# Performance work log

Hardware: AMD Instinct MI355X
Metric: run time of the kernel (lower is better)

The kernel has to match this reference:

```python
import math
import jax, jax.numpy as jnp
import numpy as np

B, S, D, H = 4, 2048, 768, 8


def setup_inputs() -> dict:
    key = jax.random.key(0)
    ks = jax.random.split(key, 8)
    x = jax.random.normal(ks[0], (B, S, D), dtype=jnp.float32)
    # padding mask: True = masked position, shape [B, S, 1] as consumed by forward
    attention_mask = jax.random.randint(ks[1], (B, S, 1), 0, 2) == 1
    W_q = jax.random.normal(ks[2], (D, D), dtype=jnp.float32) * 0.02
    b_q = jax.random.normal(ks[3], (D,), dtype=jnp.float32) * 0.02
    W_v = jax.random.normal(ks[4], (D, D), dtype=jnp.float32) * 0.02
    b_v = jax.random.normal(ks[5], (D,), dtype=jnp.float32) * 0.02
    gamma = jnp.ones((D,), dtype=jnp.float32)
    beta = jnp.zeros((D,), dtype=jnp.float32)
    return {"x": x, "attention_mask": attention_mask, "W_q": W_q, "b_q": b_q,
            "W_v": W_v, "b_v": b_v, "gamma": gamma, "beta": beta}


def reference(x, attention_mask, W_q, b_q, W_v, b_v, gamma, beta):
    b, s, d = x.shape
    dk = d // H
    scale = math.sqrt(dk)
    q = (x @ W_q.T + b_q).reshape(b, s, H, dk).transpose(0, 2, 1, 3)  # [B,H,S,dk]
    # faithful to source: k and v BOTH use the V projection (original bug)
    kv = (x @ W_v.T + b_v).reshape(b, s, H, dk).transpose(0, 2, 1, 3)
    k = kv
    v = kv
    weight = jnp.einsum('bhid,bhjd->bhij', q, k) / scale  # [B,H,S,S]
    pad = attention_mask[:, None, :, :]                   # [B,1,S,1] -> broadcast over heads, j
    causal = jnp.triu(jnp.ones((s, s), dtype=bool), 1)    # [S,S]
    mask = pad | causal
    weight = jnp.where(mask, jnp.float32(-1e9), weight)
    # faithful: softmax over dim=2 (the query axis), as in the source
    score = jax.nn.softmax(weight, axis=2)
    out = jnp.einsum('bhij,bhjd->bhid', score, v)         # [B,H,S,dk]
    out = out.transpose(0, 2, 1, 3).reshape(b, s, d)
    out = out + x                                          # residual
    mu = jnp.mean(out, axis=-1, keepdims=True)
    var = jnp.mean((out - mu) ** 2, axis=-1, keepdims=True)
    return (out - mu) / jnp.sqrt(var + 1e-5) * gamma + beta
```

## Files before the change

### kernel.cpp

```cpp
#include <hip/hip_runtime.h>

#define B 4
#define S 2048
#define D 768
#define H 8
#define DK 96
#define NBH (B*H)
#define SD (B*S*D)

typedef __bf16 bf16x8 __attribute__((ext_vector_type(8)));
typedef float f32x4 __attribute__((ext_vector_type(4)));
typedef unsigned short ushort_t;
typedef __attribute__((ext_vector_type(8))) unsigned short ushort8;
typedef __attribute__((ext_vector_type(4))) unsigned short us4;

static constexpr float INV_SCALE = 0.10206207261596577f;
static constexpr float NEG = -1.0e9f;

__device__ __forceinline__ ushort_t f2bf(float f) {
    union { float f; unsigned u; } v; v.f = f;
    unsigned r = v.u + 0x7fffu + ((v.u >> 16) & 1u);
    return (ushort_t)(r >> 16);
}

__device__ __forceinline__ unsigned cvt_pk(float a, float b) {
    unsigned d;
    asm("v_cvt_pk_bf16_f32 %0, %1, %2" : "=v"(d) : "v"(a), "v"(b));
    return d;
}
__device__ __forceinline__ ushort8 pack8(const float4& a, const float4& b) {
    union { unsigned u[4]; ushort8 s; } r;
    r.u[0] = cvt_pk(a.x, a.y); r.u[1] = cvt_pk(a.z, a.w);
    r.u[2] = cvt_pk(b.x, b.y); r.u[3] = cvt_pk(b.z, b.w);
    return r.s;
}
__device__ __forceinline__ us4 pack4(const float4& a) {
    union { unsigned u[2]; us4 s; } r;
    r.u[0] = cvt_pk(a.x, a.y); r.u[1] = cvt_pk(a.z, a.w);
    return r.s;
}

#define MFMA16(a, b, c) __builtin_amdgcn_mfma_f32_16x16x32_bf16((a), (b), (c), 0, 0, 0)

__global__ __launch_bounds__(256) void convert_bf16(
    const float* __restrict__ wq, const float* __restrict__ wv,
    ushort_t* __restrict__ wqb, ushort_t* __restrict__ wvb)
{
    const int stride = gridDim.x * 256;
    const int idx = blockIdx.x * 256 + threadIdx.x;
    for (int i = idx; i < (D * D) / 4; i += stride) {
        ((us4*)wqb)[i] = pack4(((const float4*)wq)[i]);
        ((us4*)wvb)[i] = pack4(((const float4*)wv)[i]);
    }
}

__global__ __launch_bounds__(256) void in_proj_gemm(
    const float* __restrict__ x,
    const ushort_t* __restrict__ wqb, const float* __restrict__ bq,
    const ushort_t* __restrict__ wvb, const float* __restrict__ bv,
    ushort_t* __restrict__ Qb, ushort_t* __restrict__ KVb,
    ushort_t* __restrict__ KVt)
{
    const ushort_t* __restrict__ Wm = blockIdx.z ? wvb : wqb;
    const float* __restrict__ bia   = blockIdx.z ? bv : bq;
    ushort_t* __restrict__ outp     = blockIdx.z ? KVb : Qb;

    const int bn = blockIdx.x * 128;
    const int bm = blockIdx.y * 128;
    const int tid = threadIdx.x;
    const int lane = tid & 63;
    const int wid = tid >> 6;
    const int wm = (wid >> 1) * 64, wn = (wid & 1) * 64;
    const int lr = lane & 15, lg = lane >> 4;

    __shared__ __align__(16) ushort_t As[2][128][40];
    __shared__ __align__(16) ushort_t Bs[2][128][40];

    const int r0 = tid >> 2, c8 = (tid & 3) * 8;
    const float*    xg0 = &x [(size_t)(bm + r0) * D + c8];
    const float*    xg1 = xg0 + (size_t)64 * D;
    const ushort_t* wg0 = &Wm[(size_t)(bn + r0) * D + c8];
    const ushort_t* wg1 = wg0 + (size_t)64 * D;

    float4 xv[4];
    ushort8 wv2[2];

    f32x4 acc[4][4];
    #pragma unroll
    for (int m = 0; m < 4; ++m)
        #pragma unroll
        for (int n = 0; n < 4; ++n) acc[m][n] = (f32x4){0.f, 0.f, 0.f, 0.f};

    {
        xv[0] = *(const float4*)(xg0);     xv[1] = *(const float4*)(xg0 + 4);
        xv[2] = *(const float4*)(xg1);     xv[3] = *(const float4*)(xg1 + 4);
        wv2[0] = *(const ushort8*)(wg0);   wv2[1] = *(const ushort8*)(wg1);
        *(ushort8*)&As[0][r0][c8]      = pack8(xv[0], xv[1]);
        *(ushort8*)&As[0][r0 + 64][c8] = pack8(xv[2], xv[3]);
        *(ushort8*)&Bs[0][r0][c8]      = wv2[0];
        *(ushort8*)&Bs[0][r0 + 64][c8] = wv2[1];
    }

    for (int k = 0; k < 24; ++k) {
        __syncthreads();
        const int buf = k & 1;
        if (k < 23) {
            const int ko = (k + 1) * 32;
            xv[0] = *(const float4*)(xg0 + ko);     xv[1] = *(const float4*)(xg0 + ko + 4);
            xv[2] = *(const float4*)(xg1 + ko);     xv[3] = *(const float4*)(xg1 + ko + 4);
            wv2[0] = *(const ushort8*)(wg0 + ko);   wv2[1] = *(const ushort8*)(wg1 + ko);
        }
        bf16x8 a[4], bfr[4];
        #pragma unroll
        for (int m = 0; m < 4; ++m) a[m]   = *(const bf16x8*)&As[buf][wm + m * 16 + lr][lg * 8];
        #pragma unroll
        for (int n = 0; n < 4; ++n) bfr[n] = *(const bf16x8*)&Bs[buf][wn + n * 16 + lr][lg * 8];
        #pragma unroll
        for (int m = 0; m < 4; ++m)
            #pragma unroll
            for (int n = 0; n < 4; ++n)
                acc[m][n] = MFMA16(a[m], bfr[n], acc[m][n]);
        if (k < 23) {
            const int nb = (k + 1) & 1;
            *(ushort8*)&As[nb][r0][c8]      = pack8(xv[0], xv[1]);
            *(ushort8*)&As[nb][r0 + 64][c8] = pack8(xv[2], xv[3]);
            *(ushort8*)&Bs[nb][r0][c8]      = wv2[0];
            *(ushort8*)&Bs[nb][r0 + 64][c8] = wv2[1];
        }
    }

    #pragma unroll
    for (int m = 0; m < 4; ++m) {
        #pragma unroll
        for (int n = 0; n < 4; ++n) {
            int col = bn + wn + n * 16 + lr;
            float bb = bia[col];
            int row0 = bm + wm + m * 16 + lg * 4;
            us4 o;
            #pragma unroll
            for (int r = 0; r < 4; ++r) o[r] = f2bf(acc[m][n][r] + bb);
            #pragma unroll
            for (int r = 0; r < 4; ++r) outp[(size_t)(row0 + r) * D + col] = o[r];
            if (blockIdx.z) {
                int hh = col / DK, dd = col - hh * DK;
                int bb2 = row0 >> 11, ss = row0 & (S - 1);
                *(us4*)&KVt[((size_t)(bb2 * H + hh) * DK + dd) * S + ss] = o;
            }
        }
    }
}

__global__ __launch_bounds__(256) void col_stats(
    const ushort_t* __restrict__ Qb, const ushort_t* __restrict__ KVb,
    const int* __restrict__ amask,
    float* __restrict__ colM, float* __restrict__ colSinv)
{
    const int bh = blockIdx.y;
    const int jt = (blockIdx.x + 8 * ((bh >> 3) & 3)) & 31;
    const int b = bh >> 3, h = bh & 7;
    const int j0 = jt * 64;
    const int tid = threadIdx.x;
    const int lane = tid & 63;
    const int w = tid >> 6;
    const int lr = lane & 15, lg = lane >> 4;

    __shared__ __align__(16) ushort_t qs[2][64][104];
    __shared__ int pads[2][64];

    bf16x8 kf[3];
    #pragma unroll
    for (int ks2 = 0; ks2 < 3; ++ks2)
        kf[ks2] = *(const bf16x8*)&KVb[(size_t)(b * S + j0 + w * 16 + lr) * D + h * DK + ks2 * 32 + lg * 8];

    int kr[3], kc[3];
    const ushort_t* qg[3];
    #pragma unroll
    for (int k3 = 0; k3 < 3; ++k3) {
        int c = tid + k3 * 256;
        kr[k3] = c / 12; kc[k3] = (c % 12) * 8;
        qg[k3] = &Qb[(size_t)(b * S + j0 + kr[k3]) * D + h * DK + kc[k3]];
    }
    const int* pg = amask + b * S + j0 + (tid < 64 ? tid : 0);

    ushort8 pq[3]; int ppad = 0;
    #pragma unroll
    for (int k3 = 0; k3 < 3; ++k3) { pq[k3] = *(const ushort8*)qg[k3]; qg[k3] += (size_t)64 * D; }
    if (tid < 64) { ppad = *pg; }
    pg += 64;

    float m = NEG, ssum = 0.f;
    const int jg = j0 + w * 16 + lr;
    const int nit = (S / 64) - jt;

    for (int t = 0; t < nit; ++t) {
        const int buf = t & 1;
        const int i0 = j0 + t * 64;
        #pragma unroll
        for (int k3 = 0; k3 < 3; ++k3) *(ushort8*)&qs[buf][kr[k3]][kc[k3]] = pq[k3];
        if (tid < 64) pads[buf][tid] = ppad;
        __syncthreads();
        if (t + 1 < nit) {
            #pragma unroll
            for (int k3 = 0; k3 < 3; ++k3) { pq[k3] = *(const ushort8*)qg[k3]; qg[k3] += (size_t)64 * D; }
            if (tid < 64) { ppad = *pg; }
            pg += 64;
        }

        f32x4 dacc[4];
        #pragma unroll
        for (int f = 0; f < 4; ++f) dacc[f] = (f32x4){0.f, 0.f, 0.f, 0.f};
        #pragma unroll
        for (int ks2 = 0; ks2 < 3; ++ks2) {
            #pragma unroll
            for (int f = 0; f < 4; ++f) {
                bf16x8 afr = *(const bf16x8*)&qs[buf][f * 16 + lr][ks2 * 32 + lg * 8];
                dacc[f] = MFMA16(afr, kf[ks2], dacc[f]);
            }
        }

        #pragma unroll
        for (int f = 0; f < 4; ++f) {
            const int ib = f * 16 + lg * 4;
            float wv[4];
            #pragma unroll
            for (int r = 0; r < 4; ++r) {
                int ig = i0 + ib + r;
                wv[r] = (pads[buf][ib + r] != 0 || jg > ig) ? NEG : dacc[f][r] * INV_SCALE;
            }
            float vmax = fmaxf(fmaxf(wv[0], wv[1]), fmaxf(wv[2], wv[3]));
            float mn = fmaxf(m, vmax);
            ssum = ssum * __expf(m - mn)
                 + __expf(wv[0] - mn) + __expf(wv[1] - mn)
                 + __expf(wv[2] - mn) + __expf(wv[3] - mn);
            m = mn;
        }
    }

    float m2 = m, s2 = ssum;
    #pragma unroll
    for (int off = 16; off < 64; off <<= 1) {
        float mo = __shfl_xor(m2, off);
        float so = __shfl_xor(s2, off);
        float mn = fmaxf(m2, mo);
        s2 = s2 * __expf(m2 - mn) + so * __expf(mo - mn);
        m2 = mn;
    }
    if (lane < 16) {
        if (m2 == NEG) s2 += (float)j0;
        colM[bh * S + jg] = m2;
        colSinv[bh * S + jg] = 1.0f / s2;
    }
}

__global__ __launch_bounds__(256, 4) void attn_pv(
    const ushort_t* __restrict__ Qb, const ushort_t* __restrict__ KVb,
    const ushort_t* __restrict__ KVt,
    const int* __restrict__ amask,
    const float* __restrict__ colM, const float* __restrict__ colSinv,
    const float* __restrict__ x, float* __restrict__ out)
{
    const int bh = blockIdx.y;
    const int it = (blockIdx.x + 8 * ((bh >> 3) & 3)) & 31;
    const int b = bh >> 3, h = bh & 7;
    const int i0 = it * 64;
    const int tid = threadIdx.x;
    const int lane = tid & 63;
    const int w = tid >> 6;
    const int lr = lane & 15, lg = lane >> 4;

    __shared__ __align__(16) ushort_t kvs[64][104];
    __shared__ __align__(16) ushort_t kvt[96][72];
    __shared__ __align__(16) ushort_t ps[64][72];
    __shared__ __align__(16) float cm[64];
    __shared__ __align__(16) float csv[64];
    __shared__ int padi[64];

    bf16x8 qf[3];
    #pragma unroll
    for (int ks2 = 0; ks2 < 3; ++ks2)
        qf[ks2] = *(const bf16x8*)&Qb[(size_t)(b * S + i0 + w * 16 + lr) * D + h * DK + ks2 * 32 + lg * 8];

    if (tid < 64) padi[tid] = amask[b * S + i0 + tid];

    int kr[3], kc[3], tr[3], tc[3];
    const ushort_t* kvg[3];
    const ushort_t* ktg[3];
    #pragma unroll
    for (int k3 = 0; k3 < 3; ++k3) {
        int c = tid + k3 * 256;
        kr[k3] = c / 12;  kc[k3] = (c % 12) * 8;
        tr[k3] = c >> 3;  tc[k3] = (c & 7) * 8;
        kvg[k3] = &KVb[(size_t)(b * S + kr[k3]) * D + h * DK + kc[k3]];
        ktg[k3] = &KVt[((size_t)(b * H + h) * DK + tr[k3]) * S + tc[k3]];
    }
    const float* cmg  = colM    + (size_t)bh * S + (tid < 64 ? tid : 0);
    const float* csvg = colSinv + (size_t)bh * S + (tid < 64 ? tid : 0);

    ushort8 pkv[3], pkt[3]; float pcm = 0.f, pcsv = 0.f;
    #pragma unroll
    for (int k3 = 0; k3 < 3; ++k3) {
        pkv[k3] = *(const ushort8*)kvg[k3];  kvg[k3] += (size_t)64 * D;
        pkt[k3] = *(const ushort8*)ktg[k3];  ktg[k3] += 64;
    }
    if (tid < 64) { pcm = *cmg; pcsv = *csvg; }
    cmg += 64; csvg += 64;

    f32x4 acc[6];
    #pragma unroll
    for (int df = 0; df < 6; ++df) acc[df] = (f32x4){0.f, 0.f, 0.f, 0.f};

    const int my_pad = (int)(amask[b * S + i0 + w * 16 + lr] != 0);
    const int i_g = i0 + w * 16 + lr;

    for (int jt2 = 0; jt2 <= it; ++jt2) {
        const int j0 = jt2 * 64;
        __syncthreads();
        #pragma unroll
        for (int k3 = 0; k3 < 3; ++k3) {
            *(ushort8*)&kvs[kr[k3]][kc[k3]] = pkv[k3];
            *(ushort8*)&kvt[tr[k3]][tc[k3]] = pkt[k3];
        }
        if (tid < 64) { cm[tid] = pcm; csv[tid] = pcsv; }
        __syncthreads();
        if (jt2 < it) {
            #pragma unroll
            for (int k3 = 0; k3 < 3; ++k3) {
                pkv[k3] = *(const ushort8*)kvg[k3];  kvg[k3] += (size_t)64 * D;
                pkt[k3] = *(const ushort8*)ktg[k3];  ktg[k3] += 64;
            }
            if (tid < 64) { pcm = *cmg; pcsv = *csvg; }
            cmg += 64; csvg += 64;
        }

        f32x4 dacc[4];
        #pragma unroll
        for (int jf = 0; jf < 4; ++jf) dacc[jf] = (f32x4){0.f, 0.f, 0.f, 0.f};
        #pragma unroll
        for (int ks2 = 0; ks2 < 3; ++ks2) {
            #pragma unroll
            for (int jf = 0; jf < 4; ++jf) {
                bf16x8 afr = *(const bf16x8*)&kvs[jf * 16 + lr][ks2 * 32 + lg * 8];
                dacc[jf] = MFMA16(afr, qf[ks2], dacc[jf]);
            }
        }

        #pragma unroll
        for (int jf = 0; jf < 4; ++jf) {
            const int jbase = jf * 16 + lg * 4;
            f32x4 cmv  = *(const f32x4*)&cm[jbase];
            f32x4 csvv = *(const f32x4*)&csv[jbase];
            float pv[4];
            #pragma unroll
            for (int r = 0; r < 4; ++r) {
                int jgl = j0 + jbase + r;
                bool msk = my_pad || (jgl > i_g);
                float wvv = msk ? NEG : dacc[jf][r] * INV_SCALE;
                pv[r] = __expf(wvv - cmv[r]) * csvv[r];
            }
            union { unsigned u[2]; uint2 v; } o;
            o.u[0] = cvt_pk(pv[0], pv[1]);
            o.u[1] = cvt_pk(pv[2], pv[3]);
            *(uint2*)&ps[w * 16 + lr][jbase] = o.v;
        }

        #pragma unroll
        for (int ks2 = 0; ks2 < 2; ++ks2) {
            bf16x8 afr = *(const bf16x8*)&ps[w * 16 + lr][ks2 * 32 + lg * 8];
            #pragma unroll
            for (int df = 0; df < 6; ++df) {
                bf16x8 bfr = *(const bf16x8*)&kvt[df * 16 + lr][ks2 * 32 + lg * 8];
                acc[df] = MFMA16(afr, bfr, acc[df]);
            }
        }
    }

    #pragma unroll
    for (int df = 0; df < 6; ++df) {
        int d = h * DK + df * 16 + lr;
        #pragma unroll
        for (int r = 0; r < 4; ++r) {
            size_t gi = (size_t)(b * S + i0 + w * 16 + lg * 4 + r) * D + d;
            out[gi] = acc[df][r] + x[gi];
        }
    }
}

__global__ __launch_bounds__(256) void layer_norm(
    float* __restrict__ out,
    const float* __restrict__ gamma, const float* __restrict__ beta)
{
    const int row = blockIdx.x * 4 + (threadIdx.x >> 6);
    const int lane = threadIdx.x & 63;
    float* o = out + (size_t)row * D;

    float4 v[3];
    #pragma unroll
    for (int p = 0; p < 3; ++p) v[p] = *(const float4*)&o[lane * 4 + p * 256];

    float s = 0.f;
    #pragma unroll
    for (int p = 0; p < 3; ++p) s += v[p].x + v[p].y + v[p].z + v[p].w;
    #pragma unroll
    for (int off = 1; off < 64; off <<= 1) s += __shfl_xor(s, off);
    const float mu = s * (1.0f / D);

    float q = 0.f;
    #pragma unroll
    for (int p = 0; p < 3; ++p) {
        float a = v[p].x - mu, bb = v[p].y - mu, c = v[p].z - mu, dd = v[p].w - mu;
        q += a * a + bb * bb + c * c + dd * dd;
    }
    #pragma unroll
    for (int off = 1; off < 64; off <<= 1) q += __shfl_xor(q, off);
    const float inv = 1.0f / sqrtf(q * (1.0f / D) + 1e-5f);

    #pragma unroll
    for (int p = 0; p < 3; ++p) {
        float4 g = *(const float4*)&gamma[lane * 4 + p * 256];
        float4 bt = *(const float4*)&beta[lane * 4 + p * 256];
        float4 r;
        r.x = (v[p].x - mu) * inv * g.x + bt.x;
        r.y = (v[p].y - mu) * inv * g.y + bt.y;
        r.z = (v[p].z - mu) * inv * g.z + bt.z;
        r.w = (v[p].w - mu) * inv * g.w + bt.w;
        *(float4*)&o[lane * 4 + p * 256] = r;
    }
}

extern "C" void kernel_launch(void* const* d_in, const int* in_sizes, int n_in,
                              void* d_out, int out_size, void* d_ws, size_t ws_size,
                              hipStream_t stream)
{
    const float* x     = (const float*)d_in[0];
    const int*   amask = (const int*)  d_in[1];
    const float* Wq    = (const float*)d_in[2];
    const float* bq    = (const float*)d_in[3];
    const float* Wv    = (const float*)d_in[4];
    const float* bv    = (const float*)d_in[5];
    const float* gamma = (const float*)d_in[6];
    const float* beta  = (const float*)d_in[7];
    float* out = (float*)d_out;

    ushort_t* wqb  = (ushort_t*)d_ws;
    ushort_t* wvb  = wqb + (size_t)D * D;
    ushort_t* Qb   = wvb + (size_t)D * D;
    ushort_t* KVb  = Qb  + (size_t)SD;
    ushort_t* KVt  = KVb + (size_t)SD;
    float* colM    = (float*)(KVt + (size_t)SD);
    float* colSinv = colM + (size_t)NBH * S;

    convert_bf16<<<576, 256, 0, stream>>>(Wq, Wv, wqb, wvb);
    in_proj_gemm<<<dim3(D / 128, (B * S) / 128, 2), 256, 0, stream>>>(
        x, wqb, bq, wvb, bv, Qb, KVb, KVt);
    col_stats<<<dim3(S / 64, NBH), 256, 0, stream>>>(
        Qb, KVb, amask, colM, colSinv);
    attn_pv<<<dim3(S / 64, NBH), 256, 0, stream>>>(
        Qb, KVb, KVt, amask, colM, colSinv, x, out);
    layer_norm<<<(B * S) / 4, 256, 0, stream>>>(out, gamma, beta);
}
```

Baseline: 178.1 us.

## Load attention operands straight from global into registers and fold scale into Q

Both attention kernels stop staging Q/K/V tiles, mask and column stats through shared memory with double buffering and block barriers. Each wave now loads its MFMA fragments directly from global memory (relying on L2/cache reuse across waves) and drops the __syncthreads. The softmax scale times log2(e) is folded into the Q projection epilogue so the kernels use raw exp2 instead of multiply plus __expf. Launch bounds change too; the risk is redundant global traffic across the four waves and higher register pressure.

```diff
diff --git a/kernel.cpp b/kernel.cpp
--- a/kernel.cpp
+++ b/kernel.cpp
@@ -14,8 +14,10 @@
 typedef __attribute__((ext_vector_type(8))) unsigned short ushort8;
 typedef __attribute__((ext_vector_type(4))) unsigned short us4;
 
-static constexpr float INV_SCALE = 0.10206207261596577f;
 static constexpr float NEG = -1.0e9f;
+static constexpr float SCALE_L2E = 0.14724515567714155f;
+
+__device__ __forceinline__ float exp2v(float x) { return __builtin_amdgcn_exp2f(x); }
 
 __device__ __forceinline__ ushort_t f2bf(float f) {
     union { float f; unsigned u; } v; v.f = f;
@@ -64,6 +66,7 @@
     const ushort_t* __restrict__ Wm = blockIdx.z ? wvb : wqb;
     const float* __restrict__ bia   = blockIdx.z ? bv : bq;
     ushort_t* __restrict__ outp     = blockIdx.z ? KVb : Qb;
+    const float osc = blockIdx.z ? 1.0f : SCALE_L2E;
 
     const int bn = blockIdx.x * 128;
     const int bm = blockIdx.y * 128;
@@ -138,7 +141,7 @@
             int row0 = bm + wm + m * 16 + lg * 4;
             us4 o;
             #pragma unroll
-            for (int r = 0; r < 4; ++r) o[r] = f2bf(acc[m][n][r] + bb);
+            for (int r = 0; r < 4; ++r) o[r] = f2bf((acc[m][n][r] + bb) * osc);
             #pragma unroll
             for (int r = 0; r < 4; ++r) outp[(size_t)(row0 + r) * D + col] = o[r];
             if (blockIdx.z) {
@@ -150,7 +153,7 @@
     }
 }
 
-__global__ __launch_bounds__(256) void col_stats(
+__global__ __launch_bounds__(256, 4) void col_stats(
     const ushort_t* __restrict__ Qb, const ushort_t* __restrict__ KVb,
     const int* __restrict__ amask,
     float* __restrict__ colM, float* __restrict__ colSinv)
@@ -159,79 +162,61 @@
     const int jt = (blockIdx.x + 8 * ((bh >> 3) & 3)) & 31;
     const int b = bh >> 3, h = bh & 7;
     const int j0 = jt * 64;
-    const int tid = threadIdx.x;
-    const int lane = tid & 63;
-    const int w = tid >> 6;
+    const int lane = threadIdx.x & 63;
+    const int w = threadIdx.x >> 6;
     const int lr = lane & 15, lg = lane >> 4;
-
-    __shared__ __align__(16) ushort_t qs[2][64][104];
-    __shared__ int pads[2][64];
 
     bf16x8 kf[3];
     #pragma unroll
     for (int ks2 = 0; ks2 < 3; ++ks2)
         kf[ks2] = *(const bf16x8*)&KVb[(size_t)(b * S + j0 + w * 16 + lr) * D + h * DK + ks2 * 32 + lg * 8];
 
-    int kr[3], kc[3];
-    const ushort_t* qg[3];
-    #pragma unroll
-    for (int k3 = 0; k3 < 3; ++k3) {
-        int c = tid + k3 * 256;
-        kr[k3] = c / 12; kc[k3] = (c % 12) * 8;
-        qg[k3] = &Qb[(size_t)(b * S + j0 + kr[k3]) * D + h * DK + kc[k3]];
-    }
-    const int* pg = amask + b * S + j0 + (tid < 64 ? tid : 0);
-
-    ushort8 pq[3]; int ppad = 0;
-    #pragma unroll
-    for (int k3 = 0; k3 < 3; ++k3) { pq[k3] = *(const ushort8*)qg[k3]; qg[k3] += (size_t)64 * D; }
-    if (tid < 64) { ppad = *pg; }
-    pg += 64;
+    const ushort_t* qbase = &Qb[(size_t)(b * S + j0 + lr) * D + h * DK + lg * 8];
+    const int* pbase = &amask[b * S + j0 + lg * 4];
 
     float m = NEG, ssum = 0.f;
     const int jg = j0 + w * 16 + lr;
     const int nit = (S / 64) - jt;
 
     for (int t = 0; t < nit; ++t) {
-        const int buf = t & 1;
         const int i0 = j0 + t * 64;
-        #pragma unroll
-        for (int k3 = 0; k3 < 3; ++k3) *(ushort8*)&qs[buf][kr[k3]][kc[k3]] = pq[k3];
-        if (tid < 64) pads[buf][tid] = ppad;
-        __syncthreads();
-        if (t + 1 < nit) {
-            #pragma unroll
-            for (int k3 = 0; k3 < 3; ++k3) { pq[k3] = *(const ushort8*)qg[k3]; qg[k3] += (size_t)64 * D; }
-            if (tid < 64) { ppad = *pg; }
-            pg += 64;
-        }
+        const ushort_t* qt = qbase + (size_t)t * 64 * D;
+        const int* pt = pbase + t * 64;
+
+        bf16x8 af[4][3];
+        #pragma unroll
+        for (int f = 0; f < 4; ++f)
+            #pragma unroll
+            for (int ks2 = 0; ks2 < 3; ++ks2)
+                af[f][ks2] = *(const bf16x8*)(qt + (size_t)f * 16 * D + ks2 * 32);
+        int4 pd4[4];
+        #pragma unroll
+        for (int f = 0; f < 4; ++f) pd4[f] = *(const int4*)(pt + f * 16);
 
         f32x4 dacc[4];
         #pragma unroll
         for (int f = 0; f < 4; ++f) dacc[f] = (f32x4){0.f, 0.f, 0.f, 0.f};
         #pragma unroll
-        for (int ks2 = 0; ks2 < 3; ++ks2) {
-            #pragma unroll
-            for (int f = 0; f < 4; ++f) {
-                bf16x8 afr = *(const bf16x8*)&qs[buf][f * 16 + lr][ks2 * 32 + lg * 8];
-                dacc[f] = MFMA16(afr, kf[ks2], dacc[f]);
-            }
-        }
+        for (int ks2 = 0; ks2 < 3; ++ks2)
+            #pragma unroll
+            for (int f = 0; f < 4; ++f)
+                dacc[f] = MFMA16(af[f][ks2], kf[ks2], dacc[f]);
 
         #pragma unroll
         for (int f = 0; f < 4; ++f) {
             const int ib = f * 16 + lg * 4;
+            const int* pd = (const int*)&pd4[f];
             float wv[4];
             #pragma unroll
             for (int r = 0; r < 4; ++r) {
                 int ig = i0 + ib + r;
-                wv[r] = (pads[buf][ib + r] != 0 || jg > ig) ? NEG : dacc[f][r] * INV_SCALE;
+                wv[r] = (pd[r] != 0 || jg > ig) ? NEG : dacc[f][r];
             }
             float vmax = fmaxf(fmaxf(wv[0], wv[1]), fmaxf(wv[2], wv[3]));
             float mn = fmaxf(m, vmax);
-            ssum = ssum * __expf(m - mn)
-                 + __expf(wv[0] - mn) + __expf(wv[1] - mn)
-                 + __expf(wv[2] - mn) + __expf(wv[3] - mn);
+            ssum = ssum * exp2v(m - mn)
+                 + exp2v(wv[0] - mn) + exp2v(wv[1] - mn)
+                 + exp2v(wv[2] - mn) + exp2v(wv[3] - mn);
             m = mn;
         }
     }
@@ -242,7 +227,7 @@
         float mo = __shfl_xor(m2, off);
         float so = __shfl_xor(s2, off);
         float mn = fmaxf(m2, mo);
-        s2 = s2 * __expf(m2 - mn) + so * __expf(mo - mn);
+        s2 = s2 * exp2v(m2 - mn) + so * exp2v(mo - mn);
         m2 = mn;
     }
     if (lane < 16) {
@@ -252,7 +237,7 @@
     }
 }
 
-__global__ __launch_bounds__(256, 4) void attn_pv(
+__global__ __launch_bounds__(256, 3) void attn_pv(
     const ushort_t* __restrict__ Qb, const ushort_t* __restrict__ KVb,
     const ushort_t* __restrict__ KVt,
     const int* __restrict__ amask,
@@ -263,99 +248,73 @@
     const int it = (blockIdx.x + 8 * ((bh >> 3) & 3)) & 31;
     const int b = bh >> 3, h = bh & 7;
     const int i0 = it * 64;
-    const int tid = threadIdx.x;
-    const int lane = tid & 63;
-    const int w = tid >> 6;
+    const int lane = threadIdx.x & 63;
+    const int w = threadIdx.x >> 6;
     const int lr = lane & 15, lg = lane >> 4;
 
-    __shared__ __align__(16) ushort_t kvs[64][104];
-    __shared__ __align__(16) ushort_t kvt[96][72];
     __shared__ __align__(16) ushort_t ps[64][72];
-    __shared__ __align__(16) float cm[64];
-    __shared__ __align__(16) float csv[64];
-    __shared__ int padi[64];
 
     bf16x8 qf[3];
     #pragma unroll
     for (int ks2 = 0; ks2 < 3; ++ks2)
         qf[ks2] = *(const bf16x8*)&Qb[(size_t)(b * S + i0 + w * 16 + lr) * D + h * DK + ks2 * 32 + lg * 8];
 
-    if (tid < 64) padi[tid] = amask[b * S + i0 + tid];
-
-    int kr[3], kc[3], tr[3], tc[3];
-    const ushort_t* kvg[3];
-    const ushort_t* ktg[3];
-    #pragma unroll
-    for (int k3 = 0; k3 < 3; ++k3) {
-        int c = tid + k3 * 256;
-        kr[k3] = c / 12;  kc[k3] = (c % 12) * 8;
-        tr[k3] = c >> 3;  tc[k3] = (c & 7) * 8;
-        kvg[k3] = &KVb[(size_t)(b * S + kr[k3]) * D + h * DK + kc[k3]];
-        ktg[k3] = &KVt[((size_t)(b * H + h) * DK + tr[k3]) * S + tc[k3]];
-    }
-    const float* cmg  = colM    + (size_t)bh * S + (tid < 64 ? tid : 0);
-    const float* csvg = colSinv + (size_t)bh * S + (tid < 64 ? tid : 0);
-
-    ushort8 pkv[3], pkt[3]; float pcm = 0.f, pcsv = 0.f;
-    #pragma unroll
-    for (int k3 = 0; k3 < 3; ++k3) {
-        pkv[k3] = *(const ushort8*)kvg[k3];  kvg[k3] += (size_t)64 * D;
-        pkt[k3] = *(const ushort8*)ktg[k3];  ktg[k3] += 64;
-    }
-    if (tid < 64) { pcm = *cmg; pcsv = *csvg; }
-    cmg += 64; csvg += 64;
-
-    f32x4 acc[6];
-    #pragma unroll
-    for (int df = 0; df < 6; ++df) acc[df] = (f32x4){0.f, 0.f, 0.f, 0.f};
-
     const int my_pad = (int)(amask[b * S + i0 + w * 16 + lr] != 0);
     const int i_g = i0 + w * 16 + lr;
 
+    const ushort_t* kbase = &KVb[(size_t)(b * S + lr) * D + h * DK + lg * 8];
+    const ushort_t* vbase = &KVt[((size_t)(b * H + h) * DK + lr) * S + lg * 8];
+    const float* cmb  = colM    + (size_t)bh * S + lg * 4;
+    const float* csvb = colSinv + (size_t)bh * S + lg * 4;
+
+    f32x4 acc[6];
+    #pragma unroll
+    for (int df = 0; df < 6; ++df) acc[df] = (f32x4){0.f, 0.f, 0.f, 0.f};
+
     for (int jt2 = 0; jt2 <= it; ++jt2) {
         const int j0 = jt2 * 64;
-        __syncthreads();
-        #pragma unroll
-        for (int k3 = 0; k3 < 3; ++k3) {
-            *(ushort8*)&kvs[kr[k3]][kc[k3]] = pkv[k3];
-            *(ushort8*)&kvt[tr[k3]][tc[k3]] = pkt[k3];
-        }
-        if (tid < 64) { cm[tid] = pcm; csv[tid] = pcsv; }
-        __syncthreads();
-        if (jt2 < it) {
-            #pragma unroll
-            for (int k3 = 0; k3 < 3; ++k3) {
-                pkv[k3] = *(const ushort8*)kvg[k3];  kvg[k3] += (size_t)64 * D;
-                pkt[k3] = *(const ushort8*)ktg[k3];  ktg[k3] += 64;
-            }
-            if (tid < 64) { pcm = *cmg; pcsv = *csvg; }
-            cmg += 64; csvg += 64;
+        const ushort_t* kt = kbase + (size_t)j0 * D;
+        const ushort_t* vt = vbase + j0;
+
+        bf16x8 kf[4][3];
+        #pragma unroll
+        for (int jf = 0; jf < 4; ++jf)
+            #pragma unroll
+            for (int ks2 = 0; ks2 < 3; ++ks2)
+                kf[jf][ks2] = *(const bf16x8*)(kt + (size_t)jf * 16 * D + ks2 * 32);
+
+        bf16x8 vf[6][2];
+        #pragma unroll
+        for (int df = 0; df < 6; ++df)
+            #pragma unroll
+            for (int ks2 = 0; ks2 < 2; ++ks2)
+                vf[df][ks2] = *(const bf16x8*)(vt + (size_t)df * 16 * S + ks2 * 32);
+        f32x4 cmv[4], csvv[4];
+        #pragma unroll
+        for (int jf = 0; jf < 4; ++jf) {
+            cmv[jf]  = *(const f32x4*)(cmb  + j0 + jf * 16);
+            csvv[jf] = *(const f32x4*)(csvb + j0 + jf * 16);
         }
 
         f32x4 dacc[4];
         #pragma unroll
         for (int jf = 0; jf < 4; ++jf) dacc[jf] = (f32x4){0.f, 0.f, 0.f, 0.f};
         #pragma unroll
-        for (int ks2 = 0; ks2 < 3; ++ks2) {
-            #pragma unroll
-            for (int jf = 0; jf < 4; ++jf) {
-                bf16x8 afr = *(const bf16x8*)&kvs[jf * 16 + lr][ks2 * 32 + lg * 8];
-                dacc[jf] = MFMA16(afr, qf[ks2], dacc[jf]);
-            }
-        }
+        for (int ks2 = 0; ks2 < 3; ++ks2)
+            #pragma unroll
+            for (int jf = 0; jf < 4; ++jf)
+                dacc[jf] = MFMA16(kf[jf][ks2], qf[ks2], dacc[jf]);
 
         #pragma unroll
         for (int jf = 0; jf < 4; ++jf) {
             const int jbase = jf * 16 + lg * 4;
-            f32x4 cmv  = *(const f32x4*)&cm[jbase];
-            f32x4 csvv = *(const f32x4*)&csv[jbase];
             float pv[4];
             #pragma unroll
             for (int r = 0; r < 4; ++r) {
                 int jgl = j0 + jbase + r;
                 bool msk = my_pad || (jgl > i_g);
-                float wvv = msk ? NEG : dacc[jf][r] * INV_SCALE;
-                pv[r] = __expf(wvv - cmv[r]) * csvv[r];
+                float wvv = msk ? NEG : dacc[jf][r];
+                pv[r] = exp2v(wvv - cmv[jf][r]) * csvv[jf][r];
             }
             union { unsigned u[2]; uint2 v; } o;
             o.u[0] = cvt_pk(pv[0], pv[1]);
@@ -367,10 +326,8 @@
         for (int ks2 = 0; ks2 < 2; ++ks2) {
             bf16x8 afr = *(const bf16x8*)&ps[w * 16 + lr][ks2 * 32 + lg * 8];
             #pragma unroll
-            for (int df = 0; df < 6; ++df) {
-                bf16x8 bfr = *(const bf16x8*)&kvt[df * 16 + lr][ks2 * 32 + lg * 8];
-                acc[df] = MFMA16(afr, bfr, acc[df]);
-            }
+            for (int df = 0; df < 6; ++df)
+                acc[df] = MFMA16(afr, vf[df][ks2], acc[df]);
         }
     }
 
```

Measured after the change: 411.8 us. 2.31x slower.
